# Optimization experiments

Hardware: AMD Instinct MI355X
Metric: run time of the kernel (lower is better)

The kernel has to match this reference:

```python
import jax, jax.numpy as jnp
import numpy as np

HIDDEN = 512
HEADS = 8
HEAD_DIM = HIDDEN // HEADS   # 64
MAN_DIM = 256                # manifold_dim = hidden_dim // 2
SCALE = HEAD_DIM ** -0.5


def _c(re, im):
    return jax.lax.complex(re, im)


def setup_inputs() -> dict:
    key = jax.random.key(0)
    ks = jax.random.split(key, 13)
    def w(k, shape, fan_in):
        return (jax.random.normal(k, shape, dtype=jnp.float32) / np.sqrt(fan_in)).astype(jnp.float32)
    B, S = 2, 2048
    return {
        "x": jax.random.normal(ks[0], (B, S, HIDDEN), dtype=jnp.float32),
        "Wq_re": w(ks[1], (HIDDEN, HIDDEN), HIDDEN), "Wq_im": w(ks[2], (HIDDEN, HIDDEN), HIDDEN),
        "Wk_re": w(ks[3], (HIDDEN, HIDDEN), HIDDEN), "Wk_im": w(ks[4], (HIDDEN, HIDDEN), HIDDEN),
        "Wv_re": w(ks[5], (HIDDEN, HIDDEN), HIDDEN), "Wv_im": w(ks[6], (HIDDEN, HIDDEN), HIDDEN),
        "Wm_re": w(ks[7], (HEAD_DIM, MAN_DIM), HEAD_DIM), "Wm_im": w(ks[8], (HEAD_DIM, MAN_DIM), HEAD_DIM),
        "Wmi_re": w(ks[9], (MAN_DIM, HEAD_DIM), MAN_DIM), "Wmi_im": w(ks[10], (MAN_DIM, HEAD_DIM), MAN_DIM),
        "Wo_re": w(ks[11], (HIDDEN, HIDDEN), HIDDEN), "Wo_im": w(ks[12], (HIDDEN, HIDDEN), HIDDEN),
    }


def reference(x, Wq_re, Wq_im, Wk_re, Wk_im, Wv_re, Wv_im,
              Wm_re, Wm_im, Wmi_re, Wmi_im, Wo_re, Wo_im):
    B, S, D = x.shape
    # quantum state preparation: cast to complex, L2-normalize along last dim
    xc = x.astype(jnp.complex64)
    norm = jnp.linalg.norm(xc, axis=-1, keepdims=True)
    xc = xc / norm

    Wq, Wk, Wv = _c(Wq_re, Wq_im), _c(Wk_re, Wk_im), _c(Wv_re, Wv_im)
    Wm, Wmi, Wo = _c(Wm_re, Wm_im), _c(Wmi_re, Wmi_im), _c(Wo_re, Wo_im)

    def heads(t):  # [B,S,D] -> [B,H,S,head_dim]
        return t.reshape(B, S, HEADS, HEAD_DIM).transpose(0, 2, 1, 3)

    q = heads(xc @ Wq)
    k = heads(xc @ Wk)
    v = heads(xc @ Wv)

    # project each head onto the manifold (complex linear)
    qm = jnp.einsum('bhsd,dm->bhsm', q, Wm)
    km = jnp.einsum('bhsd,dm->bhsm', k, Wm)
    vm = jnp.einsum('bhsd,dm->bhsm', v, Wm)

    # Hermitian inner product attention scores; softmax over real part
    scores = jnp.einsum('bhqm,bhkm->bhqk', qm, jnp.conj(km)) * SCALE
    attn = jax.nn.softmax(scores.real, axis=-1).astype(jnp.complex64)

    outm = jnp.einsum('bhqk,bhkm->bhqm', attn, vm)
    out = jnp.einsum('bhsm,md->bhsd', outm, Wmi)        # back to head_dim
    out = out.transpose(0, 2, 1, 3).reshape(B, S, D)    # merge heads
    out = out @ Wo
    # return real/imag stacked as float32 (complex64 output -> [B,S,D,2])
    return jnp.stack([out.real, out.imag], axis=-1)
```

## Files before the change

kernel.cpp:

```cpp
#include <hip/hip_runtime.h>
#include <hip/hip_bf16.h>
#include <stdint.h>


typedef __attribute__((ext_vector_type(8))) short bf16x8;
typedef __attribute__((ext_vector_type(4))) float f32x4;

#define QSCALE 0.18033688011112042f

__device__ __forceinline__ unsigned short f2b(float f) {
    union { float f; unsigned int u; } v; v.f = f;
    unsigned int r = v.u + 0x7fffu + ((v.u >> 16) & 1u);
    return (unsigned short)(r >> 16);
}

__device__ __forceinline__ float b2f(short s) {
    union { float f; unsigned int u; } v;
    v.u = ((unsigned int)(unsigned short)s) << 16;
    return v.f;
}

__device__ __forceinline__ unsigned int cvtpk(float a, float b) {
    union { __hip_bfloat162 h; unsigned int u; } v;
    v.h = __float22bfloat162_rn(make_float2(a, b));
    return v.u;
}

__device__ __forceinline__ void ld16(void* lds, const void* g) {
    __builtin_amdgcn_global_load_lds(
        (__attribute__((address_space(1))) unsigned int*)(g),
        (__attribute__((address_space(3))) unsigned int*)(lds), 16, 0, 0);
}

__global__ __launch_bounds__(256) void k_prep(
        const float* __restrict__ x, unsigned short* __restrict__ xn,
        const float* __restrict__ s0, const float* __restrict__ s1,
        const float* __restrict__ s2, const float* __restrict__ s3,
        const float* __restrict__ s4, const float* __restrict__ s5,
        const float* __restrict__ s6, const float* __restrict__ s7,
        float* __restrict__ d0, float* __restrict__ d1,
        float* __restrict__ d2, float* __restrict__ d3,
        float* __restrict__ d4, float* __restrict__ d5,
        float* __restrict__ d6, float* __restrict__ d7) {
    __shared__ float tile[64][65];
    if (blockIdx.x < 1024) {
        int row  = blockIdx.x * 4 + (threadIdx.x >> 6);
        int lane = threadIdx.x & 63;
        const float4* xr = (const float4*)(x + (size_t)row * 512);
        float4 a = xr[lane], b = xr[lane + 64];
        float s = a.x*a.x + a.y*a.y + a.z*a.z + a.w*a.w
                + b.x*b.x + b.y*b.y + b.z*b.z + b.w*b.w;
        #pragma unroll
        for (int m = 1; m < 64; m <<= 1) s += __shfl_xor(s, m, 64);
        float inv = 1.0f / sqrtf(s);
        ushort4 o;
        o.x = f2b(a.x*inv); o.y = f2b(a.y*inv); o.z = f2b(a.z*inv); o.w = f2b(a.w*inv);
        *(ushort4*)&xn[(size_t)row*512 + lane*4] = o;
        o.x = f2b(b.x*inv); o.y = f2b(b.y*inv); o.z = f2b(b.z*inv); o.w = f2b(b.w*inv);
        *(ushort4*)&xn[(size_t)row*512 + 256 + lane*4] = o;
        return;
    }
    int bid = blockIdx.x - 1024;
    const float* src; float* dst; int R, C, tr, tc;
    if (bid < 384) {
        int mat = bid >> 6, tl = bid & 63;
        src = (mat==0)?s0:(mat==1)?s1:(mat==2)?s2:(mat==3)?s3:(mat==4)?s4:s5;
        dst = (mat==0)?d0:(mat==1)?d1:(mat==2)?d2:(mat==3)?d3:(mat==4)?d4:d5;
        R = 512; C = 512; tr = tl >> 3; tc = tl & 7;
    } else {
        int mat = (bid - 384) >> 2, tl = (bid - 384) & 3;
        src = mat ? s7 : s6; dst = mat ? d7 : d6;
        R = 64; C = 256; tr = 0; tc = tl;
    }
    int r0 = tr * 64, c0 = tc * 64;
    int tx = threadIdx.x & 63, ty = threadIdx.x >> 6;
    #pragma unroll
    for (int i = 0; i < 16; i++) {
        int r = ty + i*4;
        tile[r][tx] = src[(size_t)(r0 + r)*C + c0 + tx];
    }
    __syncthreads();
    #pragma unroll
    for (int i = 0; i < 16; i++) {
        int r = ty + i*4;
        dst[(size_t)(c0 + r)*R + r0 + tx] = tile[tx][r];
    }
}

__global__ __launch_bounds__(256) void k_gh(const float* __restrict__ Wm_re, const float* __restrict__ Wm_im,
                                            const float* __restrict__ WmT_re, const float* __restrict__ WmT_im,
                                            const float* __restrict__ Wmi_re, const float* __restrict__ Wmi_im,
                                            float* __restrict__ GH) {
    int id = blockIdx.x * 256 + threadIdx.x;
    int mat = id >> 12;
    int a = (id >> 6) & 63, c = id & 63;
    float s = 0.f;
    if (mat < 2) {
        for (int m = 0; m < 256; m++) {
            float ar = Wm_re[a*256+m], ai = Wm_im[a*256+m];
            float br = WmT_re[m*64+c], bi = WmT_im[m*64+c];
            s += (mat == 0) ? (ar*br + ai*bi) : (ai*br - ar*bi);
        }
        GH[id] = s;
    } else {
        for (int m = 0; m < 256; m++) {
            float ar = Wm_re[a*256+m], ai = Wm_im[a*256+m];
            float br = Wmi_re[m*64+c], bi = Wmi_im[m*64+c];
            s += (mat == 2) ? (ar*br - ai*bi) : (ar*bi + ai*br);
        }
        GH[mat*4096 + c*64 + a] = s;
    }
}

__global__ __launch_bounds__(256) void k_pack(
        const float* __restrict__ WqT_re, const float* __restrict__ WqT_im,
        const float* __restrict__ WkT_re, const float* __restrict__ WkT_im,
        const float* __restrict__ WvT_re, const float* __restrict__ WvT_im,
        const float* __restrict__ Wo_re,  const float* __restrict__ Wo_im,
        const float* __restrict__ GH,
        unsigned short* __restrict__ WqkvT, unsigned short* __restrict__ Wbig) {
    if (blockIdx.x < 6144) {
        int id = blockIdx.x * 256 + threadIdx.x;
        int n = id >> 9, k = id & 511;
        float val;
        if (n < 1024) {
            int h = n >> 7, part = (n >> 6) & 1, j = n & 63;
            const float* Gr = GH;
            const float* Gi = GH + 4096;
            const float* qr = WqT_re + (size_t)(h*64)*512 + k;
            const float* qi = WqT_im + (size_t)(h*64)*512 + k;
            float s = 0.f;
            if (part == 0) { for (int d = 0; d < 64; d++) s += qr[d*512]*Gr[d*64+j] - qi[d*512]*Gi[d*64+j]; }
            else           { for (int d = 0; d < 64; d++) s += qr[d*512]*Gi[d*64+j] + qi[d*512]*Gr[d*64+j]; }
            val = s * QSCALE;
        } else if (n < 2048) {
            int m = n - 1024; int h = m >> 7, part = (m >> 6) & 1, j = m & 63;
            val = (part ? WkT_im : WkT_re)[(size_t)(h*64+j)*512 + k];
        } else {
            int m = n - 2048; int h = m >> 7, part = (m >> 6) & 1, j = m & 63;
            val = (part ? WvT_im : WvT_re)[(size_t)(h*64+j)*512 + k];
        }
        WqkvT[id] = f2b(val);
    } else {
        int id = (blockIdx.x - 6144) * 256 + threadIdx.x;
        int np = id >> 10, kk = id & 1023;
        int c = np >> 1, p = np & 1;
        int h = kk >> 7, pp = (kk >> 6) & 1, d = kk & 63;
        const float* HrT = GH + 2*4096;
        const float* HiT = GH + 3*4096;
        float s = 0.f;
        if (p == pp) {
            for (int j = 0; j < 64; j++) {
                float hr = HrT[j*64+d], hi = HiT[j*64+d];
                float wr = Wo_re[(size_t)(h*64+j)*512 + c];
                float wi = Wo_im[(size_t)(h*64+j)*512 + c];
                s += hr*wr - hi*wi;
            }
        } else {
            for (int j = 0; j < 64; j++) {
                float hr = HrT[j*64+d], hi = HiT[j*64+d];
                float wr = Wo_re[(size_t)(h*64+j)*512 + c];
                float wi = Wo_im[(size_t)(h*64+j)*512 + c];
                s += hr*wi + hi*wr;
            }
            if (p == 0) s = -s;
        }
        Wbig[(size_t)np*1024 + kk] = f2b(s);
    }
}

template<int MODE, int MT>
__global__ __launch_bounds__(256, 2) void k_gemm(
        const unsigned short* __restrict__ Ain, const unsigned short* __restrict__ Btin,
        void* __restrict__ Cout, unsigned short* __restrict__ Vt, int K) {
    __shared__ __align__(16) unsigned short Al[MT*32];
    __shared__ __align__(16) unsigned short Bl[128*32];
    const int t = threadIdx.x;
    const int wave = t >> 6, lane = t & 63, quad = lane >> 4, l16 = lane & 15;
    const int wr = wave >> 1, wc = wave & 1;

    const unsigned short* A;
    const unsigned short* Bt;
    unsigned short* Cb = nullptr;
    int m0, n0;
    if (MODE == 0) {
        if (blockIdx.y < 16) {
            A = Ain; Bt = Btin;
            m0 = blockIdx.x * 128; n0 = blockIdx.y * 128;
            Cb = (unsigned short*)Cout;
        } else {
            int idx = (blockIdx.y - 16) * 32 + blockIdx.x;
            int b = idx >> 7, mt = (idx >> 4) & 7, nt = idx & 15;
            A  = Btin + 2048*512;
            Bt = Ain + (size_t)b*2048*512;
            m0 = mt * 128; n0 = nt * 128;
            Cb = Vt + (size_t)b*1024*2048;
        }
    } else {
        A = Ain; Bt = Btin;
        m0 = blockIdx.x * MT; n0 = blockIdx.y * 128;
    }

    f32x4 acc[MT/32][4] = {};
    for (int kt = 0; kt < K; kt += 32) {
        #pragma unroll
        for (int i = 0; i < MT/64; i++) {
            int g = t + i*256, r = g >> 2, gr = g & 3;
            ld16(&Al[g*8], &A[(size_t)(m0 + r)*K + kt + gr*8]);
        }
        #pragma unroll
        for (int i = 0; i < 2; i++) {
            int g = t + i*256, r = g >> 2, gr = g & 3;
            ld16(&Bl[g*8], &Bt[(size_t)(n0 + r)*K + kt + gr*8]);
        }
        __syncthreads();
        bf16x8 af[MT/32], bfr[4];
        #pragma unroll
        for (int rt = 0; rt < MT/32; rt++)
            af[rt] = *(const bf16x8*)&Al[(wr*(MT/2) + rt*16 + l16)*32 + quad*8];
        #pragma unroll
        for (int ct = 0; ct < 4; ct++)
            bfr[ct] = *(const bf16x8*)&Bl[(wc*64 + ct*16 + l16)*32 + quad*8];
        #pragma unroll
        for (int rt = 0; rt < MT/32; rt++)
            #pragma unroll
            for (int ct = 0; ct < 4; ct++)
                acc[rt][ct] = __builtin_amdgcn_mfma_f32_16x16x32_bf16(af[rt], bfr[ct], acc[rt][ct], 0, 0, 0);
        __syncthreads();
    }
    #pragma unroll
    for (int rt = 0; rt < MT/32; rt++) {
        int row = m0 + wr*(MT/2) + rt*16 + quad*4;
        #pragma unroll
        for (int ct = 0; ct < 4; ct++) {
            int col = n0 + wc*64 + ct*16 + l16;
            if (MODE == 0) {
                unsigned int u01 = cvtpk(acc[rt][ct][0], acc[rt][ct][1]);
                unsigned int u23 = cvtpk(acc[rt][ct][2], acc[rt][ct][3]);
                Cb[(size_t)(row+0)*2048 + col] = (unsigned short)(u01);
                Cb[(size_t)(row+1)*2048 + col] = (unsigned short)(u01 >> 16);
                Cb[(size_t)(row+2)*2048 + col] = (unsigned short)(u23);
                Cb[(size_t)(row+3)*2048 + col] = (unsigned short)(u23 >> 16);
            } else {
                float* C = (float*)Cout;
                #pragma unroll
                for (int r = 0; r < 4; r++)
                    C[(size_t)(row + r)*1024 + col] = acc[rt][ct][r];
            }
        }
    }
}

__global__ __launch_bounds__(256, 3) void k_attn(
        const unsigned short* __restrict__ QK,
        const unsigned short* __restrict__ Vt,
        unsigned short* __restrict__ Opart,
        float* __restrict__ Lpart) {
    __shared__ __align__(16) unsigned short Kl[2][4096];
    __shared__ __align__(16) unsigned short Vl[2][4096];
    __shared__ __align__(16) unsigned short Pl[4608];

    const int t = threadIdx.x, w = t >> 6, lane = t & 63, quad = lane >> 4, l16 = lane & 15;
    const int bh = blockIdx.x, b = bh >> 3, h = bh & 7;
    const int qb = blockIdx.y >> 2, quarter = blockIdx.y & 3;
    const int tok0 = b*2048 + qb*128;
    const int key0 = quarter*512;

    bf16x8 qf[2][4];
    #pragma unroll
    for (int rt = 0; rt < 2; rt++)
        #pragma unroll
        for (int ks = 0; ks < 4; ks++)
            qf[rt][ks] = *(const bf16x8*)&QK[(size_t)(tok0 + w*32 + rt*16 + l16)*2048 + h*128 + ks*32 + quad*8];

    const unsigned short* kp = QK + (size_t)(b*2048 + key0 + ((t >> 2) & 31))*2048 + 1024 + h*128
                               + (t >> 7)*32 + (t & 3)*8;
    const unsigned short* vp = Vt + (size_t)(b*1024 + h*128 + (t >> 2))*2048 + key0 + (t & 3)*8;

    f32x4 Oacc[2][8] = {};
    float ls[2][4] = {};

    #pragma unroll
    for (int i = 0; i < 2; i++) ld16(&Kl[0][(i*256 + t)*8], kp + i*64);
    #pragma unroll
    for (int i = 0; i < 2; i++) ld16(&Vl[0][(i*256 + t)*8], vp + (size_t)i*64*2048);
    __syncthreads();

    for (int it = 0; it < 16; it++) {
        const int cur = it & 1;
        if (it < 15) {
            int kt2 = (it + 1) * 32;
            #pragma unroll
            for (int i = 0; i < 2; i++) ld16(&Kl[cur^1][(i*256 + t)*8], kp + (size_t)kt2*2048 + i*64);
            #pragma unroll
            for (int i = 0; i < 2; i++) ld16(&Vl[cur^1][(i*256 + t)*8], vp + kt2 + (size_t)i*64*2048);
        }

        f32x4 S[2][2] = {};
        #pragma unroll
        for (int ks = 0; ks < 4; ks++) {
            #pragma unroll
            for (int ct = 0; ct < 2; ct++) {
                bf16x8 kf = *(const bf16x8*)&Kl[cur][ks*1024 + (ct*16 + l16)*32 + quad*8];
                #pragma unroll
                for (int rt = 0; rt < 2; rt++)
                    S[rt][ct] = __builtin_amdgcn_mfma_f32_16x16x32_bf16(qf[rt][ks], kf, S[rt][ct], 0, 0, 0);
            }
        }
        #pragma unroll
        for (int rt = 0; rt < 2; rt++) {
            #pragma unroll
            for (int ct = 0; ct < 2; ct++) {
                float p0 = exp2f(S[rt][ct][0]), p1 = exp2f(S[rt][ct][1]);
                float p2 = exp2f(S[rt][ct][2]), p3 = exp2f(S[rt][ct][3]);
                ls[rt][0] += p0; ls[rt][1] += p1; ls[rt][2] += p2; ls[rt][3] += p3;
                int q = w*32 + rt*16 + quad*4;
                int base = ct*16 + l16;
                unsigned int u01 = cvtpk(p0, p1);
                unsigned int u23 = cvtpk(p2, p3);
                Pl[base + (q+0)*36] = (unsigned short)(u01);
                Pl[base + (q+1)*36] = (unsigned short)(u01 >> 16);
                Pl[base + (q+2)*36] = (unsigned short)(u23);
                Pl[base + (q+3)*36] = (unsigned short)(u23 >> 16);
            }
        }
        bf16x8 pf[2];
        #pragma unroll
        for (int rt = 0; rt < 2; rt++)
            pf[rt] = *(const bf16x8*)&Pl[(w*32 + rt*16 + l16)*36 + quad*8];
        #pragma unroll
        for (int dt = 0; dt < 8; dt++) {
            bf16x8 vf = *(const bf16x8*)&Vl[cur][(dt*16 + l16)*32 + quad*8];
            #pragma unroll
            for (int rt = 0; rt < 2; rt++)
                Oacc[rt][dt] = __builtin_amdgcn_mfma_f32_16x16x32_bf16(pf[rt], vf, Oacc[rt][dt], 0, 0, 0);
        }
        __syncthreads();
    }

    #pragma unroll
    for (int rt = 0; rt < 2; rt++)
        #pragma unroll
        for (int r = 0; r < 4; r++) {
            float s = ls[rt][r];
            #pragma unroll
            for (int m = 1; m < 16; m <<= 1) s += __shfl_xor(s, m, 64);
            ls[rt][r] = s;
        }
    unsigned short* Op = Opart + (size_t)quarter*4096*1024;
    float* Lp = Lpart + (size_t)quarter*32768;
    #pragma unroll
    for (int rt = 0; rt < 2; rt++) {
        int q = w*32 + rt*16 + quad*4;
        int tok = tok0 + q;
        float inv[4];
        #pragma unroll
        for (int r = 0; r < 4; r++) inv[r] = 1.0f / ls[rt][r];
        if (l16 == 0) {
            #pragma unroll
            for (int r = 0; r < 4; r++) Lp[(size_t)(tok + r)*8 + h] = ls[rt][r];
        }
        #pragma unroll
        for (int dt = 0; dt < 8; dt++) {
            int col = h*128 + dt*16 + l16;
            #pragma unroll
            for (int r = 0; r < 4; r++)
                Op[(size_t)(tok + r)*1024 + col] = f2b(Oacc[rt][dt][r] * inv[r]);
        }
    }
}

__global__ __launch_bounds__(256) void k_merge(const unsigned short* __restrict__ Opart,
                                               const float* __restrict__ Lpart,
                                               unsigned short* __restrict__ O) {
    int slot = blockIdx.x * 256 + threadIdx.x;
    int tok = slot >> 7, colg = slot & 127, h = colg >> 4;
    float l0 = Lpart[(size_t)tok*8 + h];
    float l1 = Lpart[32768 + (size_t)tok*8 + h];
    float l2 = Lpart[65536 + (size_t)tok*8 + h];
    float l3 = Lpart[98304 + (size_t)tok*8 + h];
    float inv = 1.0f / (l0 + l1 + l2 + l3);
    float w0 = l0*inv, w1 = l1*inv, w2 = l2*inv, w3 = l3*inv;
    size_t off = (size_t)tok*1024 + colg*8;
    bf16x8 a0 = *(const bf16x8*)&Opart[off];
    bf16x8 a1 = *(const bf16x8*)&Opart[4194304 + off];
    bf16x8 a2 = *(const bf16x8*)&Opart[8388608 + off];
    bf16x8 a3 = *(const bf16x8*)&Opart[12582912 + off];
    float o[8];
    #pragma unroll
    for (int j = 0; j < 8; j++)
        o[j] = w0*b2f(a0[j]) + w1*b2f(a1[j]) + w2*b2f(a2[j]) + w3*b2f(a3[j]);
    uint4 uo;
    uo.x = cvtpk(o[0], o[1]); uo.y = cvtpk(o[2], o[3]);
    uo.z = cvtpk(o[4], o[5]); uo.w = cvtpk(o[6], o[7]);
    *(uint4*)&O[off] = uo;
}

extern "C" void kernel_launch(void* const* d_in, const int* in_sizes, int n_in,
                              void* d_out, int out_size, void* d_ws, size_t ws_size,
                              hipStream_t stream) {
    (void)in_sizes; (void)n_in; (void)out_size; (void)ws_size;
    const float* x      = (const float*)d_in[0];
    const float* Wq_re  = (const float*)d_in[1];
    const float* Wq_im  = (const float*)d_in[2];
    const float* Wk_re  = (const float*)d_in[3];
    const float* Wk_im  = (const float*)d_in[4];
    const float* Wv_re  = (const float*)d_in[5];
    const float* Wv_im  = (const float*)d_in[6];
    const float* Wm_re  = (const float*)d_in[7];
    const float* Wm_im  = (const float*)d_in[8];
    const float* Wmi_re = (const float*)d_in[9];
    const float* Wmi_im = (const float*)d_in[10];
    const float* Wo_re  = (const float*)d_in[11];
    const float* Wo_im  = (const float*)d_in[12];

    char* ws = (char*)d_ws;
    unsigned short* xn    = (unsigned short*)(ws);
    unsigned short* WqkvT = (unsigned short*)(ws + (4u << 20));
    unsigned short* Wbig  = (unsigned short*)(ws + (7u << 20));
    float*          GH    = (float*)         (ws + (9u << 20));
    float*          WmT_re= (float*)         (ws + (9u << 20) + (64u << 10));
    float*          WmT_im= (float*)         (ws + (9u << 20) + (128u << 10));
    unsigned short* QK    = (unsigned short*)(ws + (10u << 20));
    unsigned short* Vt    = (unsigned short*)(ws + (26u << 20));
    unsigned short* Obuf  = (unsigned short*)(ws + (34u << 20));
    unsigned short* Opart = (unsigned short*)(ws + (42u << 20));
    float*          Lpart = (float*)         (ws + (74u << 20));
    float* WqT_re = (float*)(ws + (10u << 20));
    float* WqT_im = (float*)(ws + (11u << 20));
    float* WkT_re = (float*)(ws + (12u << 20));
    float* WkT_im = (float*)(ws + (13u << 20));
    float* WvT_re = (float*)(ws + (14u << 20));
    float* WvT_im = (float*)(ws + (15u << 20));

    k_prep      <<<dim3(1416), dim3(256), 0, stream>>>(
        x, xn,
        Wq_re, Wq_im, Wk_re, Wk_im, Wv_re, Wv_im, Wm_re, Wm_im,
        WqT_re, WqT_im, WkT_re, WkT_im, WvT_re, WvT_im, WmT_re, WmT_im);
    k_gh        <<<dim3(64),   dim3(256), 0, stream>>>(Wm_re, Wm_im, WmT_re, WmT_im, Wmi_re, Wmi_im, GH);
    k_pack      <<<dim3(10240),dim3(256), 0, stream>>>(
        WqT_re, WqT_im, WkT_re, WkT_im, WvT_re, WvT_im, Wo_re, Wo_im, GH, WqkvT, Wbig);
    k_gemm<0,128><<<dim3(32, 24), dim3(256), 0, stream>>>(xn, WqkvT, (void*)QK, Vt, 512);
    k_attn      <<<dim3(16, 64), dim3(256), 0, stream>>>(QK, Vt, Opart, Lpart);
    k_merge     <<<dim3(2048), dim3(256), 0, stream>>>(Opart, Lpart, Obuf);
    k_gemm<1,64> <<<dim3(64, 8), dim3(256), 0, stream>>>(Obuf, Wbig, d_out, nullptr, 1024);
}
```

Baseline: 260.5 us.

## Double k-step per barrier in GEMM; load V directly to registers in attention

The GEMM now stages two 32-wide K slices per iteration, which halves the number of __syncthreads barriers. The attention kernel processes 64 keys per iteration instead of 32. It drops the V shared-memory buffer and loads V fragments straight from global memory into registers, while K stays double-buffered in LDS. These changes aim to cut barrier and LDS traffic overhead, at the cost of higher register pressure and global-latency exposure on the V loads. The Pl buffer is reused within one iteration without a barrier between the two halves, so wave-local correctness depends on each wave only reading its own rows.

```diff
diff --git a/kernel.cpp b/kernel.cpp
--- a/kernel.cpp
+++ b/kernel.cpp
@@ -173,8 +173,8 @@
 __global__ __launch_bounds__(256, 2) void k_gemm(
         const unsigned short* __restrict__ Ain, const unsigned short* __restrict__ Btin,
         void* __restrict__ Cout, unsigned short* __restrict__ Vt, int K) {
-    __shared__ __align__(16) unsigned short Al[MT*32];
-    __shared__ __align__(16) unsigned short Bl[128*32];
+    __shared__ __align__(16) unsigned short Al[2][MT*32];
+    __shared__ __align__(16) unsigned short Bl[2][128*32];
     const int t = threadIdx.x;
     const int wave = t >> 6, lane = t & 63, quad = lane >> 4, l16 = lane & 15;
     const int wr = wave >> 1, wc = wave & 1;
@@ -202,30 +202,36 @@
     }
 
     f32x4 acc[MT/32][4] = {};
-    for (int kt = 0; kt < K; kt += 32) {
-        #pragma unroll
-        for (int i = 0; i < MT/64; i++) {
-            int g = t + i*256, r = g >> 2, gr = g & 3;
-            ld16(&Al[g*8], &A[(size_t)(m0 + r)*K + kt + gr*8]);
-        }
-        #pragma unroll
-        for (int i = 0; i < 2; i++) {
-            int g = t + i*256, r = g >> 2, gr = g & 3;
-            ld16(&Bl[g*8], &Bt[(size_t)(n0 + r)*K + kt + gr*8]);
+    for (int kt = 0; kt < K; kt += 64) {
+        #pragma unroll
+        for (int kh = 0; kh < 2; kh++) {
+            #pragma unroll
+            for (int i = 0; i < MT/64; i++) {
+                int g = t + i*256, r = g >> 2, gr = g & 3;
+                ld16(&Al[kh][g*8], &A[(size_t)(m0 + r)*K + kt + kh*32 + gr*8]);
+            }
+            #pragma unroll
+            for (int i = 0; i < 2; i++) {
+                int g = t + i*256, r = g >> 2, gr = g & 3;
+                ld16(&Bl[kh][g*8], &Bt[(size_t)(n0 + r)*K + kt + kh*32 + gr*8]);
+            }
         }
         __syncthreads();
-        bf16x8 af[MT/32], bfr[4];
-        #pragma unroll
-        for (int rt = 0; rt < MT/32; rt++)
-            af[rt] = *(const bf16x8*)&Al[(wr*(MT/2) + rt*16 + l16)*32 + quad*8];
-        #pragma unroll
-        for (int ct = 0; ct < 4; ct++)
-            bfr[ct] = *(const bf16x8*)&Bl[(wc*64 + ct*16 + l16)*32 + quad*8];
-        #pragma unroll
-        for (int rt = 0; rt < MT/32; rt++)
+        #pragma unroll
+        for (int kh = 0; kh < 2; kh++) {
+            bf16x8 af[MT/32], bfr[4];
+            #pragma unroll
+            for (int rt = 0; rt < MT/32; rt++)
+                af[rt] = *(const bf16x8*)&Al[kh][(wr*(MT/2) + rt*16 + l16)*32 + quad*8];
             #pragma unroll
             for (int ct = 0; ct < 4; ct++)
-                acc[rt][ct] = __builtin_amdgcn_mfma_f32_16x16x32_bf16(af[rt], bfr[ct], acc[rt][ct], 0, 0, 0);
+                bfr[ct] = *(const bf16x8*)&Bl[kh][(wc*64 + ct*16 + l16)*32 + quad*8];
+            #pragma unroll
+            for (int rt = 0; rt < MT/32; rt++)
+                #pragma unroll
+                for (int ct = 0; ct < 4; ct++)
+                    acc[rt][ct] = __builtin_amdgcn_mfma_f32_16x16x32_bf16(af[rt], bfr[ct], acc[rt][ct], 0, 0, 0);
+        }
         __syncthreads();
     }
     #pragma unroll
@@ -256,8 +262,7 @@
         const unsigned short* __restrict__ Vt,
         unsigned short* __restrict__ Opart,
         float* __restrict__ Lpart) {
-    __shared__ __align__(16) unsigned short Kl[2][4096];
-    __shared__ __align__(16) unsigned short Vl[2][4096];
+    __shared__ __align__(16) unsigned short Kl[2][8192];
     __shared__ __align__(16) unsigned short Pl[4608];
 
     const int t = threadIdx.x, w = t >> 6, lane = t & 63, quad = lane >> 4, l16 = lane & 15;
@@ -273,40 +278,43 @@
         for (int ks = 0; ks < 4; ks++)
             qf[rt][ks] = *(const bf16x8*)&QK[(size_t)(tok0 + w*32 + rt*16 + l16)*2048 + h*128 + ks*32 + quad*8];
 
-    const unsigned short* kp = QK + (size_t)(b*2048 + key0 + ((t >> 2) & 31))*2048 + 1024 + h*128
-                               + (t >> 7)*32 + (t & 3)*8;
-    const unsigned short* vp = Vt + (size_t)(b*1024 + h*128 + (t >> 2))*2048 + key0 + (t & 3)*8;
+    const unsigned short* kp = QK + (size_t)(b*2048 + key0 + (t >> 2))*2048 + 1024 + h*128 + (t & 3)*8;
+    const unsigned short* vbase = Vt + (size_t)(b*1024 + h*128)*2048 + key0;
 
     f32x4 Oacc[2][8] = {};
     float ls[2][4] = {};
 
     #pragma unroll
-    for (int i = 0; i < 2; i++) ld16(&Kl[0][(i*256 + t)*8], kp + i*64);
-    #pragma unroll
-    for (int i = 0; i < 2; i++) ld16(&Vl[0][(i*256 + t)*8], vp + (size_t)i*64*2048);
+    for (int i = 0; i < 4; i++) ld16(&Kl[0][(i*256 + t)*8], kp + i*32);
     __syncthreads();
 
-    for (int it = 0; it < 16; it++) {
+    for (int it = 0; it < 8; it++) {
         const int cur = it & 1;
-        if (it < 15) {
-            int kt2 = (it + 1) * 32;
-            #pragma unroll
-            for (int i = 0; i < 2; i++) ld16(&Kl[cur^1][(i*256 + t)*8], kp + (size_t)kt2*2048 + i*64);
-            #pragma unroll
-            for (int i = 0; i < 2; i++) ld16(&Vl[cur^1][(i*256 + t)*8], vp + kt2 + (size_t)i*64*2048);
-        }
-
-        f32x4 S[2][2] = {};
+        const int kt = it * 64;
+
+        bf16x8 vf0[8];
+        #pragma unroll
+        for (int dt = 0; dt < 8; dt++)
+            vf0[dt] = *(const bf16x8*)&vbase[(size_t)(dt*16 + l16)*2048 + kt + quad*8];
+
+        if (it < 7) {
+            #pragma unroll
+            for (int i = 0; i < 4; i++)
+                ld16(&Kl[cur^1][(i*256 + t)*8], kp + (size_t)(kt + 64)*2048 + i*32);
+        }
+
+        f32x4 S[2][4] = {};
         #pragma unroll
         for (int ks = 0; ks < 4; ks++) {
             #pragma unroll
-            for (int ct = 0; ct < 2; ct++) {
-                bf16x8 kf = *(const bf16x8*)&Kl[cur][ks*1024 + (ct*16 + l16)*32 + quad*8];
+            for (int ct = 0; ct < 4; ct++) {
+                bf16x8 kf = *(const bf16x8*)&Kl[cur][ks*2048 + (ct*16 + l16)*32 + quad*8];
                 #pragma unroll
                 for (int rt = 0; rt < 2; rt++)
                     S[rt][ct] = __builtin_amdgcn_mfma_f32_16x16x32_bf16(qf[rt][ks], kf, S[rt][ct], 0, 0, 0);
             }
         }
+
         #pragma unroll
         for (int rt = 0; rt < 2; rt++) {
             #pragma unroll
@@ -324,16 +332,51 @@
                 Pl[base + (q+3)*36] = (unsigned short)(u23 >> 16);
             }
         }
-        bf16x8 pf[2];
-        #pragma unroll
-        for (int rt = 0; rt < 2; rt++)
-            pf[rt] = *(const bf16x8*)&Pl[(w*32 + rt*16 + l16)*36 + quad*8];
-        #pragma unroll
-        for (int dt = 0; dt < 8; dt++) {
-            bf16x8 vf = *(const bf16x8*)&Vl[cur][(dt*16 + l16)*32 + quad*8];
+        {
+            bf16x8 pf[2];
             #pragma unroll
             for (int rt = 0; rt < 2; rt++)
-                Oacc[rt][dt] = __builtin_amdgcn_mfma_f32_16x16x32_bf16(pf[rt], vf, Oacc[rt][dt], 0, 0, 0);
+                pf[rt] = *(const bf16x8*)&Pl[(w*32 + rt*16 + l16)*36 + quad*8];
+            #pragma unroll
+            for (int dt = 0; dt < 8; dt++)
+                #pragma unroll
+                for (int rt = 0; rt < 2; rt++)
+                    Oacc[rt][dt] = __builtin_amdgcn_mfma_f32_16x16x32_bf16(pf[rt], vf0[dt], Oacc[rt][dt], 0, 0, 0);
+        }
+
+        bf16x8 vf1[8];
+        #pragma unroll
+        for (int dt = 0; dt < 8; dt++)
+            vf1[dt] = *(const bf16x8*)&vbase[(size_t)(dt*16 + l16)*2048 + kt + 32 + quad*8];
+
+        #pragma unroll
+        for (int rt = 0; rt < 2; rt++) {
+            #pragma unroll
+            for (int ct2 = 0; ct2 < 2; ct2++) {
+                int ct = 2 + ct2;
+                float p0 = exp2f(S[rt][ct][0]), p1 = exp2f(S[rt][ct][1]);
+                float p2 = exp2f(S[rt][ct][2]), p3 = exp2f(S[rt][ct][3]);
+                ls[rt][0] += p0; ls[rt][1] += p1; ls[rt][2] += p2; ls[rt][3] += p3;
+                int q = w*32 + rt*16 + quad*4;
+                int base = ct2*16 + l16;
+                unsigned int u01 = cvtpk(p0, p1);
+                unsigned int u23 = cvtpk(p2, p3);
+                Pl[base + (q+0)*36] = (unsigned short)(u01);
+                Pl[base + (q+1)*36] = (unsigned short)(u01 >> 16);
+                Pl[base + (q+2)*36] = (unsigned short)(u23);
+                Pl[base + (q+3)*36] = (unsigned short)(u23 >> 16);
+            }
+        }
+        {
+            bf16x8 pf[2];
+            #pragma unroll
+            for (int rt = 0; rt < 2; rt++)
+                pf[rt] = *(const bf16x8*)&Pl[(w*32 + rt*16 + l16)*36 + quad*8];
+            #pragma unroll
+            for (int dt = 0; dt < 8; dt++)
+                #pragma unroll
+                for (int rt = 0; rt < 2; rt++)
+                    Oacc[rt][dt] = __builtin_amdgcn_mfma_f32_16x16x32_bf16(pf[rt], vf1[dt], Oacc[rt][dt], 0, 0, 0);
         }
         __syncthreads();
     }
```

New measurement: 329.0 us. 26.3% more time.
